# Performance work log

Measured on AMD Instinct MI355X. Metric: run time of the kernel, lower is better.

## Reference

```python
import jax, jax.numpy as jnp
import numpy as np

B, S, E, H, D = 4, 2048, 1024, 8, 256  # batch, seq, embed_dim, heads, hidden_units


def setup_inputs() -> dict:
    key = jax.random.key(0)
    ks = jax.random.split(key, 9)
    scale = 0.02
    return {
        "inputA": jax.random.normal(ks[0], (B, S, E), dtype=jnp.float32),
        "WQ": jax.random.normal(ks[1], (H, E, D), dtype=jnp.float32) * scale,
        "bQ": jnp.zeros((H, D), dtype=jnp.float32),
        "WK": jax.random.normal(ks[2], (H, E, D), dtype=jnp.float32) * scale,
        "bK": jnp.zeros((H, D), dtype=jnp.float32),
        "WV": jax.random.normal(ks[3], (H, E, D), dtype=jnp.float32) * scale,
        "bV": jnp.zeros((H, D), dtype=jnp.float32),
        "WZ": jax.random.normal(ks[4], (H * D, E), dtype=jnp.float32) * scale,
        "bZ": jnp.zeros((E,), dtype=jnp.float32),
    }


def reference(inputA, WQ, bQ, WK, bK, WV, bV, WZ, bZ):
    # Per-head Linear -> ReLU (dropout=0 -> identity); heads stacked on axis h.
    Q = jax.nn.relu(jnp.einsum('bse,hed->bhsd', inputA, WQ) + bQ[None, :, None, :])
    K = jax.nn.relu(jnp.einsum('bse,hed->bhsd', inputA, WK) + bK[None, :, None, :])
    V = jax.nn.relu(jnp.einsum('bse,hed->bhsd', inputA, WV) + bV[None, :, None, :])
    # scores[b,h,s,t] ; torch bmm output was [B, S, T] per head
    scores = jnp.einsum('bhsd,bhtd->bhst', Q, K) / jnp.sqrt(jnp.float32(E))
    # double softmax: torch dim=1 (query axis s) then dim=2 (key axis t)
    A = jax.nn.softmax(scores, axis=2)
    A = jax.nn.softmax(A, axis=3)
    Z = jnp.einsum('bhst,bhtd->bhsd', A, V)
    # concat heads along feature dim (head order matches torch cat)
    Zall = Z.transpose(0, 2, 1, 3).reshape(B, S, H * D)
    return Zall @ WZ + bZ
```

## Files before the change

kernel.cpp:

```cpp
#include <hip/hip_runtime.h>

typedef __attribute__((ext_vector_type(8))) short short8;
typedef __attribute__((ext_vector_type(4))) float f32x4;

constexpr int B_ = 4, S_ = 2048, E_ = 1024, H_ = 8, D_ = 256;
constexpr int HD_ = H_ * D_;
constexpr int BS_ = B_ * S_;
constexpr int BH_ = B_ * H_;
constexpr float C1_ = 0.04508422002778011f;
constexpr float LOG2E_ = 1.4426950408889634f;

__device__ __forceinline__ unsigned short f2bf(float f) {
    union { float f; unsigned u; } x; x.f = f;
    unsigned r = (x.u + 0x7fffu + ((x.u >> 16) & 1u)) >> 16;
    return (unsigned short)r;
}

__device__ __forceinline__ unsigned pk2(float a, float b) {
    return (unsigned)f2bf(a) | ((unsigned)f2bf(b) << 16);
}

__device__ __forceinline__ void gl_lds16(const void* g, void* lds) {
    __builtin_amdgcn_global_load_lds((const __attribute__((address_space(1))) void*)g,
                                     (__attribute__((address_space(3))) void*)lds, 16, 0, 0);
}

__global__ __launch_bounds__(256) void cast_k(const float* __restrict__ src,
                                              unsigned short* __restrict__ dst, int n4) {
    int i = blockIdx.x * 256 + threadIdx.x;
    if (i >= n4) return;
    float4 v = reinterpret_cast<const float4*>(src)[i];
    ushort4 o;
    o.x = f2bf(v.x); o.y = f2bf(v.y); o.z = f2bf(v.z); o.w = f2bf(v.w);
    reinterpret_cast<ushort4*>(dst)[i] = o;
}

__global__ __launch_bounds__(256) void tcast_k(const float* __restrict__ src,
                                               unsigned short* __restrict__ dst, int R, int C) {
    __shared__ float tile[32][33];
    int b = blockIdx.z;
    const float* s = src + (size_t)b * R * C;
    unsigned short* d = dst + (size_t)b * R * C;
    int c0 = blockIdx.x * 32, r0 = blockIdx.y * 32;
    int tx = threadIdx.x, ty = threadIdx.y;
#pragma unroll
    for (int i = 0; i < 4; ++i)
        tile[ty + i * 8][tx] = s[(size_t)(r0 + ty + i * 8) * C + c0 + tx];
    __syncthreads();
#pragma unroll
    for (int i = 0; i < 4; ++i)
        d[(size_t)(c0 + ty + i * 8) * R + r0 + tx] = f2bf(tile[tx][ty + i * 8]);
}

__global__ __launch_bounds__(256) void tbf_k(const unsigned short* __restrict__ src,
                                             unsigned short* __restrict__ dst) {
    __shared__ unsigned short tile[32][33];
    int bh = blockIdx.z;
    int d0 = blockIdx.x * 32, s0 = blockIdx.y * 32;
    int tx = threadIdx.x, ty = threadIdx.y;
#pragma unroll
    for (int i = 0; i < 4; ++i)
        tile[ty + i * 8][tx] = src[((size_t)bh * S_ + s0 + ty + i * 8) * D_ + d0 + tx];
    __syncthreads();
#pragma unroll
    for (int i = 0; i < 4; ++i)
        dst[((size_t)bh * D_ + d0 + ty + i * 8) * S_ + s0 + tx] = tile[tx][ty + i * 8];
}

__global__ __launch_bounds__(512, 2) void gemm_qkv256_k(const unsigned short* __restrict__ A,
                                                        const unsigned short* __restrict__ Bt,
                                                        const float* __restrict__ bias,
                                                        unsigned short* __restrict__ out) {
    __shared__ __align__(16) unsigned short As[2][256 * 64];
    __shared__ __align__(16) unsigned short Bs[2][256 * 64];
    const int tid = threadIdx.x;
    const int wave = tid >> 6, lane = tid & 63;
    const int quad = lane >> 4, l15 = lane & 15;
    const int wm = wave >> 2, wn = wave & 3;
    const int lrow = lane >> 3, lc = lane & 7;
    const int p = blockIdx.x;
    const int n0 = (p & 7) * 256;
    const int m0 = (p >> 3) * 256;
    int aoff[4], boff[4];
#pragma unroll
    for (int i = 0; i < 4; ++i) {
        int rA = m0 + (wave * 4 + i) * 8 + lrow;
        int rB = n0 + (wave * 4 + i) * 8 + lrow;
        aoff[i] = rA * E_ + (lc ^ lrow) * 8;
        boff[i] = rB * E_ + (lc ^ lrow) * 8;
    }
    f32x4 acc[8][4] = {};
#pragma unroll
    for (int i = 0; i < 4; ++i) {
        gl_lds16(A + aoff[i], (char*)As + (wave * 4 + i) * 1024);
        gl_lds16(Bt + boff[i], (char*)Bs + (wave * 4 + i) * 1024);
    }
    __syncthreads();
    const int v0 = (quad ^ (l15 & 7)) * 16;
    const int arow = (wm * 128 + l15) * 128;
    const int brow = (wn * 64 + l15) * 128;
    for (int k0 = 0; k0 < E_; k0 += 64) {
        const int cur = (k0 >> 6) & 1;
        if (k0 + 64 < E_) {
            char* An = (char*)As + (cur ^ 1) * 32768;
            char* Bn = (char*)Bs + (cur ^ 1) * 32768;
#pragma unroll
            for (int i = 0; i < 4; ++i) {
                gl_lds16(A + aoff[i] + k0 + 64, An + (wave * 4 + i) * 1024);
                gl_lds16(Bt + boff[i] + k0 + 64, Bn + (wave * 4 + i) * 1024);
            }
        }
        const char* Ac = (const char*)As + cur * 32768;
        const char* Bc = (const char*)Bs + cur * 32768;
#pragma unroll
        for (int kcc = 0; kcc < 2; ++kcc) {
            const int vk = v0 ^ (kcc << 6);
            short8 af[8], bf[4];
#pragma unroll
            for (int fm = 0; fm < 8; ++fm)
                af[fm] = *(const short8*)(Ac + arow + fm * 2048 + vk);
#pragma unroll
            for (int fn = 0; fn < 4; ++fn)
                bf[fn] = *(const short8*)(Bc + brow + fn * 2048 + vk);
#pragma unroll
            for (int fm = 0; fm < 8; ++fm)
#pragma unroll
                for (int fn = 0; fn < 4; ++fn)
                    acc[fm][fn] = __builtin_amdgcn_mfma_f32_16x16x32_bf16(af[fm], bf[fn], acc[fm][fn], 0, 0, 0);
        }
        __syncthreads();
    }
#pragma unroll
    for (int fm = 0; fm < 8; ++fm) {
        int mbase = m0 + wm * 128 + fm * 16 + quad * 4;
#pragma unroll
        for (int fn = 0; fn < 4; ++fn) {
            int n = n0 + wn * 64 + fn * 16 + l15;
            int h = n >> 8, d = n & 255;
            float bv = bias[n];
#pragma unroll
            for (int r = 0; r < 4; ++r) {
                int m = mbase + r;
                int b = m >> 11, s = m & 2047;
                float v = fmaxf(acc[fm][fn][r] + bv, 0.0f);
                out[((size_t)(b * H_ + h) * S_ + s) * D_ + d] = f2bf(v);
            }
        }
    }
}

__global__ __launch_bounds__(256) void gemm_out_k(const unsigned short* __restrict__ A,
                                                  const unsigned short* __restrict__ Bt,
                                                  const float* __restrict__ bias,
                                                  float* __restrict__ out) {
    __shared__ __align__(16) unsigned short As[128 * 32];
    __shared__ __align__(16) unsigned short Bs[128 * 32];
    const int tid = threadIdx.x;
    const int wave = tid >> 6, lane = tid & 63;
    const int quad = lane >> 4, l15 = lane & 15;
    const int wm = wave >> 1, wn = wave & 1;
    const int m0 = blockIdx.y * 128, n0 = blockIdx.x * 128;
    const int c1 = tid, c2 = tid + 256;
    const int r1 = c1 >> 2, kc1 = (c1 & 3) * 8;
    const int r2 = c2 >> 2, kc2 = (c2 & 3) * 8;
    char* aB1 = (char*)As + wave * 1024; char* aB2 = aB1 + 4096;
    char* bB1 = (char*)Bs + wave * 1024; char* bB2 = bB1 + 4096;
    const unsigned short* a1 = A + (size_t)(m0 + r1) * HD_ + kc1;
    const unsigned short* a2 = A + (size_t)(m0 + r2) * HD_ + kc2;
    const unsigned short* b1 = Bt + (size_t)(n0 + r1) * HD_ + kc1;
    const unsigned short* b2 = Bt + (size_t)(n0 + r2) * HD_ + kc2;
    f32x4 acc[4][4] = {};
    for (int k0 = 0; k0 < HD_; k0 += 32) {
        __syncthreads();
        gl_lds16(a1 + k0, aB1);
        gl_lds16(a2 + k0, aB2);
        gl_lds16(b1 + k0, bB1);
        gl_lds16(b2 + k0, bB2);
        __syncthreads();
        short8 af[4], bf[4];
        const short* Ass = (const short*)As;
        const short* Bss = (const short*)Bs;
#pragma unroll
        for (int f = 0; f < 4; ++f) {
            af[f] = *(const short8*)&Ass[(wm * 64 + f * 16 + l15) * 32 + quad * 8];
            bf[f] = *(const short8*)&Bss[(wn * 64 + f * 16 + l15) * 32 + quad * 8];
        }
#pragma unroll
        for (int fm = 0; fm < 4; ++fm)
#pragma unroll
            for (int fn = 0; fn < 4; ++fn)
                acc[fm][fn] = __builtin_amdgcn_mfma_f32_16x16x32_bf16(af[fm], bf[fn], acc[fm][fn], 0, 0, 0);
    }
#pragma unroll
    for (int fm = 0; fm < 4; ++fm) {
        int mbase = m0 + wm * 64 + fm * 16 + quad * 4;
#pragma unroll
        for (int fn = 0; fn < 4; ++fn) {
            int n = n0 + wn * 64 + fn * 16 + l15;
            float bv = bias[n];
#pragma unroll
            for (int r = 0; r < 4; ++r)
                out[(size_t)(mbase + r) * E_ + n] = acc[fm][fn][r] + bv;
        }
    }
}

__global__ __launch_bounds__(512, 2) void colsum_k(const unsigned short* __restrict__ Q,
                                                   const unsigned short* __restrict__ K,
                                                   float* __restrict__ invLcol) {
    __shared__ float part[8][64];
    const int tid = threadIdx.x;
    const int wave = tid >> 6, lane = tid & 63;
    const int quad = lane >> 4, l15 = lane & 15;
    const int tg = wave >> 2, sg = wave & 3;
    const int p = blockIdx.x;
    const int bh = (p & 7) + 8 * ((p >> 3) >> 4);
    const int t0 = ((p >> 3) & 15) * 128;
    const unsigned short* Qh = Q + (size_t)bh * S_ * D_;
    const unsigned short* Kh = K + (size_t)bh * S_ * D_;
    short8 kf[32];
#pragma unroll
    for (int kc = 0; kc < 8; ++kc)
#pragma unroll
        for (int fm = 0; fm < 4; ++fm)
            kf[kc * 4 + fm] = *(const short8*)&Kh[(size_t)(t0 + tg * 64 + fm * 16 + l15) * D_ + kc * 32 + quad * 8];
    float rl[4][4] = {};
    const unsigned short* Qw = Qh + (size_t)(sg * 16 + l15) * D_ + quad * 8;
    short8 qf[8];
#pragma unroll
    for (int kc = 0; kc < 8; ++kc) qf[kc] = *(const short8*)&Qw[kc * 32];
    for (int s0 = 0; s0 < S_; s0 += 64) {
        f32x4 acc[4] = {};
#pragma unroll
        for (int kc = 0; kc < 8; ++kc)
#pragma unroll
            for (int fm = 0; fm < 4; ++fm)
                acc[fm] = __builtin_amdgcn_mfma_f32_16x16x32_bf16(kf[kc * 4 + fm], qf[kc], acc[fm], 0, 0, 0);
        int sn = (s0 + 64) & (S_ - 1);
#pragma unroll
        for (int kc = 0; kc < 8; ++kc)
            qf[kc] = *(const short8*)&Qw[(size_t)sn * D_ + kc * 32];
#pragma unroll
        for (int fm = 0; fm < 4; ++fm)
#pragma unroll
            for (int r = 0; r < 4; ++r)
                rl[fm][r] += exp2f(acc[fm][r] * C1_);
    }
#pragma unroll
    for (int fm = 0; fm < 4; ++fm)
#pragma unroll
        for (int r = 0; r < 4; ++r) {
            float v = rl[fm][r];
            v += __shfl_xor(v, 1); v += __shfl_xor(v, 2);
            v += __shfl_xor(v, 4); v += __shfl_xor(v, 8);
            if (l15 == 0) part[wave][fm * 16 + quad * 4 + r] = v;
        }
    __syncthreads();
    if (tid < 128) {
        int tg2 = tid >> 6, i = tid & 63;
        float s = part[tg2 * 4 + 0][i] + part[tg2 * 4 + 1][i] +
                  part[tg2 * 4 + 2][i] + part[tg2 * 4 + 3][i];
        invLcol[(size_t)bh * S_ + t0 + tid] = LOG2E_ / s;
    }
}

__global__ __launch_bounds__(256, 2) void flash13_k(const unsigned short* __restrict__ Q,
                                                    const unsigned short* __restrict__ K,
                                                    const unsigned short* __restrict__ Vt,
                                                    const float* __restrict__ invLcol,
                                                    unsigned short* __restrict__ Zall) {
    __shared__ __align__(16) char KsB[2 * 16 * 1024];
    __shared__ __align__(16) char VsB[2 * 16 * 1024];
    const int tid = threadIdx.x;
    const int wave = tid >> 6, lane = tid & 63;
    const int q = lane >> 4, l15 = lane & 15;
    const int p = blockIdx.x;
    const int bh = (p & 7) + 8 * ((p >> 3) >> 4);
    const int s0 = ((p >> 3) & 15) * 128;
    const int bb = bh >> 3, hh = bh & 7;
    const unsigned short* Qh = Q + (size_t)bh * S_ * D_;
    const unsigned short* Kh = K + (size_t)bh * S_ * D_;
    const unsigned short* Vh = Vt + (size_t)bh * D_ * S_;
    const float* Lc = invLcol + (size_t)bh * S_;
    const int sbase = s0 + wave * 32;
    const int krow = 8 * (l15 >> 2) + (l15 & 3);

    const unsigned short* Qw0 = Qh + (size_t)(sbase + l15) * D_ + q * 8;
    const unsigned short* Qw1 = Qw0 + (size_t)16 * D_;
    short8 qreg0[8], qreg1[8];
#pragma unroll
    for (int kc = 0; kc < 8; ++kc) {
        qreg0[kc] = *(const short8*)&Qw0[kc * 32];
        qreg1[kc] = *(const short8*)&Qw1[kc * 32];
    }

    f32x4 zacc[2][16] = {};
    float rsacc[2] = {0.f, 0.f};

#pragma unroll
    for (int i = 0; i < 4; ++i) {
        const int seg = wave * 4 + i;
        const int kc = seg >> 1, sub = seg & 1;
        gl_lds16(Kh + (size_t)(sub * 4 + krow) * D_ + kc * 32 + q * 8, KsB + seg * 1024);
        gl_lds16(Vh + (size_t)(seg * 16 + l15) * S_ + q * 8, VsB + seg * 1024);
    }
    __syncthreads();

    for (int c = 0; c < 64; ++c) {
        const int t0 = c * 32;
        const char* Kcur = KsB + (c & 1) * 16384;
        const char* Vcur = VsB + (c & 1) * 16384;
        if (c < 63) {
            const int tn = t0 + 32;
            char* Knxt = KsB + ((c & 1) ^ 1) * 16384;
            char* Vnxt = VsB + ((c & 1) ^ 1) * 16384;
#pragma unroll
            for (int i = 0; i < 4; ++i) {
                const int seg = wave * 4 + i;
                const int kc = seg >> 1, sub = seg & 1;
                gl_lds16(Kh + (size_t)(tn + sub * 4 + krow) * D_ + kc * 32 + q * 8, Knxt + seg * 1024);
                gl_lds16(Vh + (size_t)(seg * 16 + l15) * S_ + tn + q * 8, Vnxt + seg * 1024);
            }
        }
        f32x4 acc[2][2] = {};
#pragma unroll
        for (int kc = 0; kc < 8; ++kc) {
            short8 kf0 = *(const short8*)(Kcur + (kc * 2 + 0) * 1024 + lane * 16);
            short8 kf1 = *(const short8*)(Kcur + (kc * 2 + 1) * 1024 + lane * 16);
            acc[0][0] = __builtin_amdgcn_mfma_f32_16x16x32_bf16(kf0, qreg0[kc], acc[0][0], 0, 0, 0);
            acc[0][1] = __builtin_amdgcn_mfma_f32_16x16x32_bf16(kf1, qreg0[kc], acc[0][1], 0, 0, 0);
            acc[1][0] = __builtin_amdgcn_mfma_f32_16x16x32_bf16(kf0, qreg1[kc], acc[1][0], 0, 0, 0);
            acc[1][1] = __builtin_amdgcn_mfma_f32_16x16x32_bf16(kf1, qreg1[kc], acc[1][1], 0, 0, 0);
        }
        const float4 iv0 = *(const float4*)(Lc + t0 + 8 * q);
        const float4 iv1 = *(const float4*)(Lc + t0 + 8 * q + 4);
        short8 pa[2];
#pragma unroll
        for (int st = 0; st < 2; ++st) {
            const f32x4 a0 = acc[st][0], a1 = acc[st][1];
            float e0 = exp2f(exp2f(a0[0] * C1_) * iv0.x);
            float e1 = exp2f(exp2f(a0[1] * C1_) * iv0.y);
            float e2 = exp2f(exp2f(a0[2] * C1_) * iv0.z);
            float e3 = exp2f(exp2f(a0[3] * C1_) * iv0.w);
            float e4 = exp2f(exp2f(a1[0] * C1_) * iv1.x);
            float e5 = exp2f(exp2f(a1[1] * C1_) * iv1.y);
            float e6 = exp2f(exp2f(a1[2] * C1_) * iv1.z);
            float e7 = exp2f(exp2f(a1[3] * C1_) * iv1.w);
            rsacc[st] += ((e0 + e1) + (e2 + e3)) + ((e4 + e5) + (e6 + e7));
            union { short8 v; unsigned u[4]; } P;
            P.u[0] = pk2(e0, e1);
            P.u[1] = pk2(e2, e3);
            P.u[2] = pk2(e4, e5);
            P.u[3] = pk2(e6, e7);
            pa[st] = P.v;
        }
#pragma unroll
        for (int dt = 0; dt < 16; ++dt) {
            short8 vb = *(const short8*)(Vcur + dt * 1024 + lane * 16);
            zacc[0][dt] = __builtin_amdgcn_mfma_f32_16x16x32_bf16(pa[0], vb, zacc[0][dt], 0, 0, 0);
            zacc[1][dt] = __builtin_amdgcn_mfma_f32_16x16x32_bf16(pa[1], vb, zacc[1][dt], 0, 0, 0);
        }
        __syncthreads();
    }
#pragma unroll
    for (int st = 0; st < 2; ++st) {
        float rs = rsacc[st];
        rs += __shfl_xor(rs, 16);
        rs += __shfl_xor(rs, 32);
#pragma unroll
        for (int r = 0; r < 4; ++r) {
            const float inv = 1.0f / __shfl(rs, q * 4 + r);
            const size_t rowoff = (size_t)(bb * S_ + sbase + st * 16 + q * 4 + r) * HD_ + hh * D_;
#pragma unroll
            for (int dt = 0; dt < 16; ++dt)
                Zall[rowoff + dt * 16 + l15] = f2bf(zacc[st][dt][r] * inv);
        }
    }
}

extern "C" void kernel_launch(void* const* d_in, const int* in_sizes, int n_in,
                              void* d_out, int out_size, void* d_ws, size_t ws_size,
                              hipStream_t stream) {
    const float* Ain = (const float*)d_in[0];
    const float* WQ = (const float*)d_in[1];
    const float* bQ = (const float*)d_in[2];
    const float* WK = (const float*)d_in[3];
    const float* bK = (const float*)d_in[4];
    const float* WV = (const float*)d_in[5];
    const float* bV = (const float*)d_in[6];
    const float* WZ = (const float*)d_in[7];
    const float* bZ = (const float*)d_in[8];
    float* out = (float*)d_out;

    char* ws = (char*)d_ws;
    size_t off = 0;
    auto alloc = [&](size_t bytes) {
        char* p = ws + off;
        off += (bytes + 255) & ~(size_t)255;
        return p;
    };
    unsigned short* Abf = (unsigned short*)alloc((size_t)BS_ * E_ * 2);
    unsigned short* Wqt = (unsigned short*)alloc((size_t)H_ * D_ * E_ * 2);
    unsigned short* Wkt = (unsigned short*)alloc((size_t)H_ * D_ * E_ * 2);
    unsigned short* Wvt = (unsigned short*)alloc((size_t)H_ * D_ * E_ * 2);
    unsigned short* Wzt = (unsigned short*)alloc((size_t)E_ * HD_ * 2);
    unsigned short* Qb = (unsigned short*)alloc((size_t)BH_ * S_ * D_ * 2);
    unsigned short* Kb = (unsigned short*)alloc((size_t)BH_ * S_ * D_ * 2);
    unsigned short* Vb = (unsigned short*)alloc((size_t)BH_ * S_ * D_ * 2);
    unsigned short* Vtb = (unsigned short*)alloc((size_t)BH_ * S_ * D_ * 2);
    unsigned short* Zb = (unsigned short*)alloc((size_t)BS_ * HD_ * 2);
    float* Lc = (float*)alloc((size_t)BH_ * S_ * 4);

    dim3 tb(32, 8);
    cast_k<<<(BS_ * E_ / 4 + 255) / 256, 256, 0, stream>>>(Ain, Abf, BS_ * E_ / 4);
    tcast_k<<<dim3(D_ / 32, E_ / 32, H_), tb, 0, stream>>>(WQ, Wqt, E_, D_);
    tcast_k<<<dim3(D_ / 32, E_ / 32, H_), tb, 0, stream>>>(WK, Wkt, E_, D_);
    tcast_k<<<dim3(D_ / 32, E_ / 32, H_), tb, 0, stream>>>(WV, Wvt, E_, D_);
    tcast_k<<<dim3(E_ / 32, HD_ / 32, 1), tb, 0, stream>>>(WZ, Wzt, HD_, E_);

    gemm_qkv256_k<<<dim3((BS_ / 256) * (HD_ / 256)), 512, 0, stream>>>(Abf, Wqt, bQ, Qb);
    gemm_qkv256_k<<<dim3((BS_ / 256) * (HD_ / 256)), 512, 0, stream>>>(Abf, Wkt, bK, Kb);
    gemm_qkv256_k<<<dim3((BS_ / 256) * (HD_ / 256)), 512, 0, stream>>>(Abf, Wvt, bV, Vb);

    tbf_k<<<dim3(D_ / 32, S_ / 32, BH_), tb, 0, stream>>>(Vb, Vtb);

    colsum_k<<<dim3(BH_ * S_ / 128), 512, 0, stream>>>(Qb, Kb, Lc);
    flash13_k<<<dim3(BH_ * S_ / 128), 256, 0, stream>>>(Qb, Kb, Vtb, Lc, Zb);

    gemm_out_k<<<dim3(E_ / 128, BS_ / 128), 256, 0, stream>>>(Zb, Wzt, bZ, out);
}
```

Before: 641.7 us.

## Rewrite output GEMM with 256x128 double-buffered swizzled tiles; use packed bf16 convert

```diff
diff --git a/kernel.cpp b/kernel.cpp
--- a/kernel.cpp
+++ b/kernel.cpp
@@ -14,10 +14,6 @@
     union { float f; unsigned u; } x; x.f = f;
     unsigned r = (x.u + 0x7fffu + ((x.u >> 16) & 1u)) >> 16;
     return (unsigned short)r;
-}
-
-__device__ __forceinline__ unsigned pk2(float a, float b) {
-    return (unsigned)f2bf(a) | ((unsigned)f2bf(b) << 16);
 }
 
 __device__ __forceinline__ void gl_lds16(const void* g, void* lds) {
@@ -149,47 +145,73 @@
     }
 }
 
-__global__ __launch_bounds__(256) void gemm_out_k(const unsigned short* __restrict__ A,
-                                                  const unsigned short* __restrict__ Bt,
-                                                  const float* __restrict__ bias,
-                                                  float* __restrict__ out) {
-    __shared__ __align__(16) unsigned short As[128 * 32];
-    __shared__ __align__(16) unsigned short Bs[128 * 32];
+__global__ __launch_bounds__(512, 2) void gemm_out256_k(const unsigned short* __restrict__ A,
+                                                        const unsigned short* __restrict__ Bt,
+                                                        const float* __restrict__ bias,
+                                                        float* __restrict__ out) {
+    __shared__ __align__(16) unsigned short As[2][256 * 64];
+    __shared__ __align__(16) unsigned short Bs[2][128 * 64];
     const int tid = threadIdx.x;
     const int wave = tid >> 6, lane = tid & 63;
     const int quad = lane >> 4, l15 = lane & 15;
     const int wm = wave >> 1, wn = wave & 1;
-    const int m0 = blockIdx.y * 128, n0 = blockIdx.x * 128;
-    const int c1 = tid, c2 = tid + 256;
-    const int r1 = c1 >> 2, kc1 = (c1 & 3) * 8;
-    const int r2 = c2 >> 2, kc2 = (c2 & 3) * 8;
-    char* aB1 = (char*)As + wave * 1024; char* aB2 = aB1 + 4096;
-    char* bB1 = (char*)Bs + wave * 1024; char* bB2 = bB1 + 4096;
-    const unsigned short* a1 = A + (size_t)(m0 + r1) * HD_ + kc1;
-    const unsigned short* a2 = A + (size_t)(m0 + r2) * HD_ + kc2;
-    const unsigned short* b1 = Bt + (size_t)(n0 + r1) * HD_ + kc1;
-    const unsigned short* b2 = Bt + (size_t)(n0 + r2) * HD_ + kc2;
+    const int lrow = lane >> 3, lc = lane & 7;
+    const int p = blockIdx.x;
+    const int n0 = (p & 7) * 128;
+    const int m0 = (p >> 3) * 256;
+    int aoff[4], boff[2];
+#pragma unroll
+    for (int i = 0; i < 4; ++i) {
+        int rA = m0 + (wave * 4 + i) * 8 + lrow;
+        aoff[i] = rA * HD_ + (lc ^ lrow) * 8;
+    }
+#pragma unroll
+    for (int i = 0; i < 2; ++i) {
+        int rB = n0 + (wave * 2 + i) * 8 + lrow;
+        boff[i] = rB * HD_ + (lc ^ lrow) * 8;
+    }
     f32x4 acc[4][4] = {};
-    for (int k0 = 0; k0 < HD_; k0 += 32) {
+#pragma unroll
+    for (int i = 0; i < 4; ++i)
+        gl_lds16(A + aoff[i], (char*)As + (wave * 4 + i) * 1024);
+#pragma unroll
+    for (int i = 0; i < 2; ++i)
+        gl_lds16(Bt + boff[i], (char*)Bs + (wave * 2 + i) * 1024);
+    __syncthreads();
+    const int v0 = (quad ^ (l15 & 7)) * 16;
+    const int arow = (wm * 64 + l15) * 128;
+    const int brow = (wn * 64 + l15) * 128;
+    for (int k0 = 0; k0 < HD_; k0 += 64) {
+        const int cur = (k0 >> 6) & 1;
+        if (k0 + 64 < HD_) {
+            char* An = (char*)As + (cur ^ 1) * 32768;
+            char* Bn = (char*)Bs + (cur ^ 1) * 16384;
+#pragma unroll
+            for (int i = 0; i < 4; ++i)
+                gl_lds16(A + aoff[i] + k0 + 64, An + (wave * 4 + i) * 1024);
+#pragma unroll
+            for (int i = 0; i < 2; ++i)
+                gl_lds16(Bt + boff[i] + k0 + 64, Bn + (wave * 2 + i) * 1024);
+        }
+        const char* Ac = (const char*)As + cur * 32768;
+        const char* Bc = (const char*)Bs + cur * 16384;
+#pragma unroll
+        for (int kcc = 0; kcc < 2; ++kcc) {
+            const int vk = v0 ^ (kcc << 6);
+            short8 af[4], bf[4];
+#pragma unroll
+            for (int fm = 0; fm < 4; ++fm)
+                af[fm] = *(const short8*)(Ac + arow + fm * 2048 + vk);
+#pragma unroll
+            for (int fn = 0; fn < 4; ++fn)
+                bf[fn] = *(const short8*)(Bc + brow + fn * 2048 + vk);
+#pragma unroll
+            for (int fm = 0; fm < 4; ++fm)
+#pragma unroll
+                for (int fn = 0; fn < 4; ++fn)
+                    acc[fm][fn] = __builtin_amdgcn_mfma_f32_16x16x32_bf16(af[fm], bf[fn], acc[fm][fn], 0, 0, 0);
+        }
         __syncthreads();
-        gl_lds16(a1 + k0, aB1);
-        gl_lds16(a2 + k0, aB2);
-        gl_lds16(b1 + k0, bB1);
-        gl_lds16(b2 + k0, bB2);
-        __syncthreads();
-        short8 af[4], bf[4];
-        const short* Ass = (const short*)As;
-        const short* Bss = (const short*)Bs;
-#pragma unroll
-        for (int f = 0; f < 4; ++f) {
-            af[f] = *(const short8*)&Ass[(wm * 64 + f * 16 + l15) * 32 + quad * 8];
-            bf[f] = *(const short8*)&Bss[(wn * 64 + f * 16 + l15) * 32 + quad * 8];
-        }
-#pragma unroll
-        for (int fm = 0; fm < 4; ++fm)
-#pragma unroll
-            for (int fn = 0; fn < 4; ++fn)
-                acc[fm][fn] = __builtin_amdgcn_mfma_f32_16x16x32_bf16(af[fm], bf[fn], acc[fm][fn], 0, 0, 0);
     }
 #pragma unroll
     for (int fm = 0; fm < 4; ++fm) {
@@ -264,7 +286,7 @@
     }
 }
 
-__global__ __launch_bounds__(256, 2) void flash13_k(const unsigned short* __restrict__ Q,
+__global__ __launch_bounds__(256, 2) void flash14_k(const unsigned short* __restrict__ Q,
                                                     const unsigned short* __restrict__ K,
                                                     const unsigned short* __restrict__ Vt,
                                                     const float* __restrict__ invLcol,
@@ -348,10 +370,10 @@
             float e7 = exp2f(exp2f(a1[3] * C1_) * iv1.w);
             rsacc[st] += ((e0 + e1) + (e2 + e3)) + ((e4 + e5) + (e6 + e7));
             union { short8 v; unsigned u[4]; } P;
-            P.u[0] = pk2(e0, e1);
-            P.u[1] = pk2(e2, e3);
-            P.u[2] = pk2(e4, e5);
-            P.u[3] = pk2(e6, e7);
+            asm("v_cvt_pk_bf16_f32 %0, %1, %2" : "=v"(P.u[0]) : "v"(e0), "v"(e1));
+            asm("v_cvt_pk_bf16_f32 %0, %1, %2" : "=v"(P.u[1]) : "v"(e2), "v"(e3));
+            asm("v_cvt_pk_bf16_f32 %0, %1, %2" : "=v"(P.u[2]) : "v"(e4), "v"(e5));
+            asm("v_cvt_pk_bf16_f32 %0, %1, %2" : "=v"(P.u[3]) : "v"(e6), "v"(e7));
             pa[st] = P.v;
         }
 #pragma unroll
@@ -425,7 +447,7 @@
     tbf_k<<<dim3(D_ / 32, S_ / 32, BH_), tb, 0, stream>>>(Vb, Vtb);
 
     colsum_k<<<dim3(BH_ * S_ / 128), 512, 0, stream>>>(Qb, Kb, Lc);
-    flash13_k<<<dim3(BH_ * S_ / 128), 256, 0, stream>>>(Qb, Kb, Vtb, Lc, Zb);
-
-    gemm_out_k<<<dim3(E_ / 128, BS_ / 128), 256, 0, stream>>>(Zb, Wzt, bZ, out);
-}
+    flash14_k<<<dim3(BH_ * S_ / 128), 256, 0, stream>>>(Qb, Kb, Vtb, Lc, Zb);
+
+    gemm_out256_k<<<dim3((BS_ / 256) * (E_ / 128)), 512, 0, stream>>>(Zb, Wzt, bZ, out);
+}
```

Result: no change. 639.6 us (-0.3%).
